# Kernel optimization log

Measured on AMD Instinct MI355X. Metric: run time of the kernel, lower is better.

Reference implementation:

```python
import jax, jax.numpy as jnp
import numpy as np

B, T, C, D = 4, 2048, 48, 512
L = 16                    # transcript length per video (distinct labels)
K = 9                     # bdy_kernel
CS = 15                   # cs_kernel
N_TR = L - 1
N_CAND = 3 * N_TR         # candidate_mul * pt_num
WIN_LEN = int(T / L * 0.15)   # int(t / t_len * win_scale)
ALPHA, BETA, GAMMA, TEMP = 1.0, 1.0, 0.1, 0.1
LOG2 = float(np.log(2.0))

def _bdy_kernel():
    ker = np.zeros((K, K), np.float32)
    c = K // 2
    ker[:c, :c] = 1; ker[c:, c:] = 1
    ker[:c, c:] = -1; ker[c:, :c] = -1
    ker[c, c] = 0
    return jnp.asarray(ker)

BDY_KER = _bdy_kernel()

def bdy_score_fn(prob):
    # prob: [T, C]; sliding windows of size K over time (zero padded)
    c = K // 2
    pad = jnp.pad(prob, ((c, c), (0, 0)))
    win = pad[jnp.arange(T)[:, None] + jnp.arange(K)[None, :]]       # [T,K,C]
    p = win[:, :, None, :]                                           # [T,K,1,C]
    m = (p + win[:, None, :, :]) / 2                                 # [T,K,K,C]
    # torch F.kl_div((m+1e-32).log(), p) = p*(log p - log(m+1e-32)), xlogy(0)=0
    kl = jnp.sum(jnp.where(p > 0, p * (jnp.log(jnp.where(p > 0, p, 1.0)) - jnp.log(m + 1e-32)), 0.0), -1)
    js = (kl + jnp.swapaxes(kl, 1, 2)) / 2
    js = -(js / LOG2 * 2 - 1)                                        # [T,K,K]
    return jnp.mean(BDY_KER[None] * js, axis=(-1, -2))               # [T]

def dp(cls_score):
    # cls_score: [N_TR, N_CAND]; min-cost alignment DP, inner jj-loop vectorized
    cost = -cls_score
    n_tr, n_x = N_TR, N_CAND
    W = 2 * n_tr + 1
    col = jnp.arange(W)
    inf = jnp.float32(jnp.inf)
    tr_at = jnp.clip(col // 2, 0, n_tr - 1)
    even = (col % 2 == 0)
    ge2 = col >= 2

    def init_cols(ii):
        c0 = jnp.where(ii < n_x - n_tr, 0.0, inf)
        c1 = jnp.where(ii <= n_x - n_tr, cost[0, ii], inf)
        d1 = jnp.where(ii <= n_x - n_tr, 1, 0).astype(jnp.int32)
        return c0, c1, d1

    c0, c1, d1 = init_cols(0)
    row0 = jnp.full((W,), inf).at[0].set(c0).at[1].set(c1)
    dir0 = jnp.zeros((W,), jnp.int32).at[1].set(d1)

    def step(prev, ii):
        dm1 = jnp.concatenate([jnp.full((1,), inf), prev[:-1]])
        dm2 = jnp.concatenate([jnp.full((2,), inf), prev[:-2]])
        c_at = cost[:, ii][tr_at]
        even_val = jnp.minimum(prev, dm1)
        even_dir = jnp.where(prev < dm1, 0, 1).astype(jnp.int32)
        odd_val = c_at + jnp.minimum(dm1, dm2)
        odd_dir = jnp.where(dm1 < dm2, 1, 2).astype(jnp.int32)
        c0, c1, d1 = init_cols(ii)
        new = jnp.where(ge2, jnp.where(even, even_val, odd_val), inf)
        new = new.at[0].set(c0).at[1].set(c1)
        dirs = jnp.where(ge2, jnp.where(even, even_dir, odd_dir), 0).astype(jnp.int32)
        dirs = dirs.at[1].set(d1)
        return new, dirs

    last, dirs = jax.lax.scan(step, row0, jnp.arange(1, n_x))
    dir_mat = jnp.concatenate([dir0[None], dirs], 0)                 # [n_x, W]
    cur_j0 = jnp.where(last[2 * n_tr] < last[2 * n_tr - 1], 2 * n_tr, 2 * n_tr - 1).astype(jnp.int32)

    def bt(cur_j, x):
        ii, dir_row = x
        is_odd = (cur_j % 2) == 1
        out_idx = jnp.where(is_odd, cur_j // 2, jnp.int32(n_tr))     # n_tr = OOB -> dropped
        new_j = cur_j - dir_row[cur_j]
        return new_j, (out_idx, ii.astype(jnp.int32))

    _, (oi, ovals) = jax.lax.scan(bt, cur_j0, (jnp.arange(n_x), dir_mat), reverse=True)
    return jnp.zeros((n_tr,), jnp.int32).at[oi].set(ovals, mode='drop')

def detect(logit, tr):
    # logit: [T,C] (detached), tr: [L] ints -> boundary frame indices [N_TR]
    prob = jax.nn.softmax(logit, -1)
    score = bdy_score_fn(prob).at[0].set(-jnp.inf)
    backup = score
    pos = jnp.arange(T)

    def pick(s, _):
        i = jnp.argmax(s)
        return jnp.where(jnp.abs(pos - i) <= WIN_LEN, -jnp.inf, s), i

    _, cand = jax.lax.scan(pick, score, None, length=N_CAND)
    cand = jnp.sort(cand)                                            # [N_CAND]
    # class-transition score at candidate points
    cc = CS // 2
    pairs = jnp.pad(prob[:, tr], ((cc, cc), (0, 0)))                 # [T+2cc, L]
    win = pairs[cand[:, None] + jnp.arange(CS)[None, :]]             # [N_CAND, CS, L]
    first, second = win[:, :, :-1], win[:, :, 1:]
    k0 = jnp.where(jnp.arange(CS) < cc, 1.0, -1.0)[None, :, None]
    cls = jnp.sum(k0 * (first - second), axis=1) / (2 * CS)          # [N_CAND, N_TR]
    cls = cls.T + backup[cand][None, :]                              # [N_TR, N_CAND]
    return cand[dp(cls)]

def _forward(tok_logit, fr_logit, vid_multi_hot, feat, mask, transcript):
    y = vid_multi_hot
    tok_loss = jnp.mean(-(y * jax.nn.log_sigmoid(tok_logit) + (1 - y) * jax.nn.log_sigmoid(-tok_logit)))
    # boundary detection on detached logits
    bdy = jax.vmap(detect)(jax.lax.stop_gradient(fr_logit), transcript)   # [B, N_TR]
    pse = jax.vmap(lambda b, tr: tr[jnp.sum(jnp.arange(T)[:, None] >= b[None, :], axis=1)])(bdy, transcript)
    # frame CE (bgw==1.0 path, full mask so no -100 labels)
    logp = jax.nn.log_softmax(fr_logit, -1)
    ce = -jnp.take_along_axis(logp, pse[..., None], axis=-1)[..., 0]
    m = mask.astype(ce.dtype)
    fr_loss = jnp.sum(ce * m) / jnp.sum(m)
    # global-local contrast
    tok_feat = jax.lax.stop_gradient(feat[:, :C, :])
    fr_feat = feat[:, C:, :]

    def glc_one(tok, fr, pse_i, tr, m_i):
        labels = jnp.sort(tr)                                        # = unique(pse[mask]), distinct labels
        oh = (pse_i[None, :] == labels[:, None]).astype(fr.dtype) * m_i[None, :]
        cnt = jnp.maximum(jnp.sum(oh, 1, keepdims=True), 1.0)
        la = (oh @ fr) / cnt
        la = la / jnp.maximum(jnp.linalg.norm(la, axis=-1, keepdims=True), 1e-12)
        tk = tok / jnp.maximum(jnp.linalg.norm(tok, axis=-1, keepdims=True), 1e-12)
        sim = (la @ tk.T) / TEMP                                     # [L, C]
        return jnp.mean(-jnp.take_along_axis(jax.nn.log_softmax(sim, -1), labels[:, None], axis=-1))

    glc_loss = jnp.mean(jax.vmap(glc_one)(tok_feat, fr_feat, pse, transcript, mask.astype(feat.dtype)))
    return ALPHA * tok_loss + BETA * fr_loss + GAMMA * glc_loss

def setup_inputs() -> dict:
    key = jax.random.key(0)
    ks = jax.random.split(key, 5)
    tok_logit = jax.random.normal(ks[0], (B, C), jnp.float32)
    fr_logit = jax.random.normal(ks[1], (B, T, C), jnp.float32)
    mask = jnp.ones((B, T), bool)
    transcript = jax.vmap(lambda k: jax.random.permutation(k, C)[:L])(jax.random.split(ks[2], B)).astype(jnp.int32)
    vid_multi_hot = jax.random.uniform(ks[3], (B, C), jnp.float32)
    feat = jax.random.normal(ks[4], (B, C + T, D), jnp.float32)
    return {"epoch": 5, "tok_logit": tok_logit, "fr_logit": fr_logit, "mask": mask,
            "transcript": transcript, "vid_multi_hot": vid_multi_hot, "feat": feat}

def reference(epoch, tok_logit, fr_logit, mask, transcript, vid_multi_hot, feat):
    # epoch >= warm_epc (=0), so the full loss path runs
    return _forward(tok_logit, fr_logit, vid_multi_hot, feat, mask, transcript)
```

## Files before the change

kernel.cpp:

```cpp
#include <hip/hip_runtime.h>
#include <math.h>

#define BB 4
#define TT 2048
#define CC 48
#define DD 512
#define LL 16
#define NTR 15
#define NCAND 45
#define WINLEN 19
#define CSW 15
#define CCHALF 7

static __device__ __forceinline__ float wave_reduce_sum(float v) {
    for (int off = 32; off; off >>= 1) v += __shfl_down(v, off);
    return v;
}

#define DPPMAX(x, ctrl) fmaxf((x), __int_as_float(__builtin_amdgcn_update_dpp( \
    __float_as_int(x), __float_as_int(x), (ctrl), 0xF, 0xF, false)))

__global__ __launch_bounds__(256) void k_lse(const float* __restrict__ fr,
                                             float* __restrict__ lse) {
    int row = blockIdx.x * 4 + (threadIdx.x >> 6);
    int lane = threadIdx.x & 63;
    float xv = (lane < CC) ? fr[(size_t)row * CC + lane] : -INFINITY;
    float m = xv;
    for (int off = 32; off; off >>= 1) m = fmaxf(m, __shfl_down(m, off));
    m = __shfl(m, 0);
    float e = (lane < CC) ? __expf(xv - m) : 0.f;
    float s = wave_reduce_sum(e);
    if (lane == 0) lse[row] = m + __logf(s);
}

__global__ __launch_bounds__(64) void k_score(const float* __restrict__ fr,
                                              const float* __restrict__ lse,
                                              float* __restrict__ score) {
    int row = blockIdx.x;
    int b = row / TT, t = row % TT;
    __shared__ float sp[9][CC];
    __shared__ float slp[9][CC];
    __shared__ float lse_s[9];
    int tid = threadIdx.x;
    if (tid < 9) {
        int r = t - 4 + tid;
        lse_s[tid] = (r >= 0 && r < TT) ? lse[b * TT + r] : 0.f;
    }
    __syncthreads();
    for (int idx = tid; idx < 9 * CC; idx += 64) {
        int i = idx / CC, c = idx - (idx / CC) * CC;
        int r = t - 4 + i;
        float pv = 0.f, lv = 0.f;
        if (r >= 0 && r < TT) {
            float x = fr[((size_t)b * TT + r) * CC + c];
            lv = x - lse_s[i];
            pv = __expf(lv);
        }
        sp[i][c] = pv;
        slp[i][c] = lv;
    }
    __syncthreads();
    float acc = 0.f;
    for (int idx = tid; idx < 4 * CC; idx += 64) {
        int i = idx / CC, c = idx - (idx / CC) * CC;
        acc += -2.f * sp[i][c] * slp[i][c];
    }
    for (int item = tid; item < 36 * CC; item += 64) {
        int pidx = item / CC, c = item - pidx * CC;
        int i = 0, rem = pidx;
        while (rem >= 8 - i) { rem -= 8 - i; ++i; }
        int j = i + 1 + rem;
        float wgt = ((i < 4) == (j < 4)) ? 1.f : -1.f;
        float pi = sp[i][c], pj = sp[j][c];
        float logm = __logf(0.5f * (pi + pj) + 1e-32f);
        acc -= wgt * (pi + pj) * logm;
    }
    acc = wave_reduce_sum(acc);
    if (tid == 0) {
        const float SC = -2.0f / (81.0f * 0.6931471805599453f);
        score[row] = (t == 0) ? -INFINITY : SC * acc;
    }
}

__global__ __launch_bounds__(256) void k_pickdp(const float* __restrict__ fr,
                                                const float* __restrict__ lse,
                                                const float* __restrict__ score,
                                                const int* __restrict__ transcript,
                                                int* __restrict__ labels_out,
                                                int* __restrict__ rowmap,
                                                float* __restrict__ fr_part,
                                                float* __restrict__ la) {
    int b = blockIdx.x;
    __shared__ int cl[NCAND];
    __shared__ float cost[NTR][NCAND];
    __shared__ int tr_s[LL];
    __shared__ int cand_s[NCAND];
    __shared__ float backup_s[NCAND];
    __shared__ signed char dir_mat[NCAND][32];
    __shared__ int bdy_s[NTR];
    __shared__ int rank_s[LL];
    __shared__ float rv[2][4];
    __shared__ int rp[2][4];
    __shared__ float redf[4];
    int tid = threadIdx.x;
    int wave = tid >> 6, lane = tid & 63;
    if (tid < LL) tr_s[tid] = transcript[b * LL + tid];

    {
        float4 z = {0.f, 0.f, 0.f, 0.f};
        float4* lz = (float4*)(la + (size_t)b * LL * DD);
        #pragma unroll
        for (int i = 0; i < LL * DD / 4 / 256; ++i) lz[i * 256 + tid] = z;
    }

    float v[8];
    {
        const float4* sp4 = (const float4*)(score + (size_t)b * TT);
        float4 va = sp4[2 * tid], vb = sp4[2 * tid + 1];
        v[0] = va.x; v[1] = va.y; v[2] = va.z; v[3] = va.w;
        v[4] = vb.x; v[5] = vb.y; v[6] = vb.z; v[7] = vb.w;
    }
    for (int it = 0; it < NCAND; ++it) {
        float best = -INFINITY; int bi = 0;
        #pragma unroll
        for (int k = 7; k >= 0; --k)
            if (v[k] >= best) { best = v[k]; bi = k; }
        int pos = tid * 8 + bi;
        float m = best;
        m = DPPMAX(m, 0x111); m = DPPMAX(m, 0x112);
        m = DPPMAX(m, 0x114); m = DPPMAX(m, 0x118);
        m = DPPMAX(m, 0x142); m = DPPMAX(m, 0x143);
        float wmax = __int_as_float(__builtin_amdgcn_readlane(__float_as_int(m), 63));
        unsigned long long ball = __ballot(best == wmax);
        int sl = (int)(__ffsll((long long)ball) - 1);
        int wpos = __builtin_amdgcn_readlane(pos, sl);
        if (lane == 0) { rv[it & 1][wave] = wmax; rp[it & 1][wave] = wpos; }
        __syncthreads();
        float bvv = -INFINITY; int mp = 0x7fffffff;
        #pragma unroll
        for (int w = 0; w < 4; ++w) {
            float vv = rv[it & 1][w]; int pp = rp[it & 1][w];
            if (vv > bvv || (vv == bvv && pp < mp)) { bvv = vv; mp = pp; }
        }
        if (tid == 0) cl[it] = mp;
        int lo = mp - WINLEN, hi = mp + WINLEN;
        #pragma unroll
        for (int k = 0; k < 8; ++k) {
            int t = tid * 8 + k;
            if (t >= lo && t <= hi) v[k] = -INFINITY;
        }
    }
    __syncthreads();
    if (tid < NCAND) {
        int my = cl[tid];
        int rank = 0;
        for (int i = 0; i < NCAND; ++i) rank += (cl[i] < my) ? 1 : 0;
        cand_s[rank] = my;
    }
    __syncthreads();
    if (tid < NCAND) backup_s[tid] = score[(size_t)b * TT + cand_s[tid]];
    __syncthreads();

    for (int e = tid; e < NTR * NCAND; e += 256) {
        int j = e / NCAND, ii = e - (e / NCAND) * NCAND;
        int cpos = cand_s[ii];
        int trj = tr_s[j], trj1 = tr_s[j + 1];
        float sum = 0.f;
        #pragma unroll
        for (int k = 0; k < CSW; ++k) {
            int r = cpos - CCHALF + k;
            float a = 0.f, d2 = 0.f;
            if (r >= 0 && r < TT) {
                size_t ro = (size_t)b * TT + r;
                float ls = lse[ro];
                a  = __expf(fr[ro * CC + trj]  - ls);
                d2 = __expf(fr[ro * CC + trj1] - ls);
            }
            sum += ((k < CCHALF) ? 1.f : -1.f) * (a - d2);
        }
        cost[j][ii] = -(sum / 30.f + backup_s[ii]);
    }
    __syncthreads();

    if (tid < 64) {
        float prev = INFINITY;
        if (tid == 0) prev = 0.f;
        if (tid == 1) prev = cost[0][0];
        if (tid < 31) dir_mat[0][tid] = (tid == 1) ? (signed char)1 : (signed char)0;
        for (int ii = 1; ii < NCAND; ++ii) {
            float dm1 = __shfl_up(prev, 1); if (tid < 1) dm1 = INFINITY;
            float dm2 = __shfl_up(prev, 2); if (tid < 2) dm2 = INFINITY;
            int trat = tid >> 1; if (trat > NTR - 1) trat = NTR - 1;
            float c_at = cost[trat][ii];
            float ev = fminf(prev, dm1);
            int ed = (prev < dm1) ? 0 : 1;
            float ov = c_at + fminf(dm1, dm2);
            int od = (dm1 < dm2) ? 1 : 2;
            float nv; int nd;
            if (tid >= 2) {
                if ((tid & 1) == 0) { nv = ev; nd = ed; }
                else { nv = ov; nd = od; }
            } else { nv = INFINITY; nd = 0; }
            if (tid == 0) { nv = (ii < NCAND - NTR) ? 0.f : INFINITY; nd = 0; }
            if (tid == 1) {
                nv = (ii <= NCAND - NTR) ? cost[0][ii] : INFINITY;
                nd = (ii <= NCAND - NTR) ? 1 : 0;
            }
            prev = nv;
            if (tid < 31) dir_mat[ii][tid] = (signed char)nd;
        }
        float v29 = __shfl(prev, 29);
        float v30 = __shfl(prev, 30);
        if (tid == 0) {
            int cur = (v30 < v29) ? 30 : 29;
            for (int ii = NCAND - 1; ii >= 0; --ii) {
                if (cur & 1) bdy_s[cur >> 1] = cand_s[ii];
                cur -= (int)dir_mat[ii][cur];
            }
        }
    }
    __syncthreads();

    if (tid < LL) {
        int myv = tr_s[tid];
        int r2 = 0;
        #pragma unroll
        for (int l2 = 0; l2 < LL; ++l2) r2 += (tr_s[l2] < myv) ? 1 : 0;
        rank_s[tid] = r2;
        labels_out[b * LL + r2] = myv;
    }
    __syncthreads();

    float facc = 0.f;
    for (int t = tid; t < TT; t += 256) {
        int cnt = 0;
        #pragma unroll
        for (int j = 0; j < NTR; ++j) cnt += (t >= bdy_s[j]) ? 1 : 0;
        int pv = tr_s[cnt];
        rowmap[b * TT + t] = rank_s[cnt];
        size_t ro = (size_t)b * TT + t;
        facc += lse[ro] - fr[ro * CC + pv];
    }
    facc = wave_reduce_sum(facc);
    if (lane == 0) redf[wave] = facc;
    __syncthreads();
    if (tid == 0) fr_part[b] = redf[0] + redf[1] + redf[2] + redf[3];
}

__global__ __launch_bounds__(256) void k_la(const float* __restrict__ feat,
                                            const int* __restrict__ rowmap,
                                            float* __restrict__ la) {
    int b = blockIdx.y;
    int t0 = blockIdx.x * 32;
    int tid = threadIdx.x;
    const float* frf = feat + ((size_t)b * (CC + TT) + CC) * DD;
    __shared__ int rm[32];
    if (tid < 32) rm[tid] = rowmap[b * TT + t0 + tid];
    __syncthreads();
    float ax = 0.f, ay = 0.f;
    int cur = rm[0];
    for (int k = 0; k < 32; ++k) {
        int r = rm[k];
        if (r != cur) {
            float* dst = la + ((size_t)b * LL + cur) * DD + tid * 2;
            atomicAdd(dst, ax);
            atomicAdd(dst + 1, ay);
            ax = 0.f; ay = 0.f; cur = r;
        }
        const float2* p = (const float2*)(frf + (size_t)(t0 + k) * DD);
        float2 v = p[tid];
        ax += v.x; ay += v.y;
    }
    float* dst = la + ((size_t)b * LL + cur) * DD + tid * 2;
    atomicAdd(dst, ax);
    atomicAdd(dst + 1, ay);
}

__global__ __launch_bounds__(256) void k_glc(const float* __restrict__ feat,
                                             const float* __restrict__ la,
                                             float* __restrict__ dots,
                                             float* __restrict__ ntk) {
    int c = blockIdx.x, b = blockIdx.y;
    __shared__ float tok_s[DD];
    __shared__ float redv[4];
    int tid = threadIdx.x;
    int wave = tid >> 6, lane = tid & 63;
    const float* tr = feat + ((size_t)b * (CC + TT) + c) * DD;
    float2 tv = ((const float2*)tr)[tid];
    ((float2*)tok_s)[tid] = tv;
    float vv = tv.x * tv.x + tv.y * tv.y;
    vv = wave_reduce_sum(vv);
    if (lane == 0) redv[wave] = vv;
    __syncthreads();
    if (tid == 0)
        ntk[b * CC + c] = fmaxf(sqrtf(redv[0] + redv[1] + redv[2] + redv[3]), 1e-12f);
    for (int l = wave; l < LL; l += 4) {
        const float4* lar = (const float4*)(la + ((size_t)b * LL + l) * DD);
        const float4* ts = (const float4*)tok_s;
        float dot = 0.f;
        #pragma unroll
        for (int jj = 0; jj < 2; ++jj) {
            int j = lane + jj * 64;
            float4 a = lar[j]; float4 w = ts[j];
            dot += a.x * w.x + a.y * w.y + a.z * w.z + a.w * w.w;
        }
        dot = wave_reduce_sum(dot);
        if (lane == 0) dots[((size_t)b * LL + l) * CC + c] = dot;
    }
}

__global__ __launch_bounds__(64) void k_term(const float* __restrict__ la,
                                             const float* __restrict__ dots,
                                             const float* __restrict__ ntk,
                                             const int* __restrict__ labels,
                                             float* __restrict__ terms) {
    int l = blockIdx.x, b = blockIdx.y;
    int lane = threadIdx.x;
    const float4* lar = (const float4*)(la + ((size_t)b * LL + l) * DD);
    float ss = 0.f;
    #pragma unroll
    for (int jj = 0; jj < 2; ++jj) {
        float4 a = lar[lane + jj * 64];
        ss += a.x * a.x + a.y * a.y + a.z * a.z + a.w * a.w;
    }
    ss = wave_reduce_sum(ss);
    float nla = fmaxf(sqrtf(__shfl(ss, 0)), 1e-12f);
    float sim = -INFINITY;
    if (lane < CC)
        sim = dots[((size_t)b * LL + l) * CC + lane] * 10.0f / (nla * ntk[b * CC + lane]);
    float mx = sim;
    for (int off = 32; off; off >>= 1) mx = fmaxf(mx, __shfl_down(mx, off));
    mx = __shfl(mx, 0);
    float e = (lane < CC) ? expf(sim - mx) : 0.f;
    float se = wave_reduce_sum(e);
    se = __shfl(se, 0);
    int lab = labels[b * LL + l];
    float sim_lab = __shfl(sim, lab);
    if (lane == 0) terms[b * LL + l] = (mx + logf(se)) - sim_lab;
}

__global__ __launch_bounds__(256) void k_combine(const float* __restrict__ tok_logit,
                                                 const float* __restrict__ vid,
                                                 const float* __restrict__ fr_part,
                                                 const float* __restrict__ terms,
                                                 float* __restrict__ out) {
    int tid = threadIdx.x;
    __shared__ float red[4];
    __shared__ float gterm;
    float acc = 0.f;
    if (tid < BB * CC) {
        float x = tok_logit[tid], y = vid[tid];
        float lsp = fminf(x, 0.f) - log1pf(expf(-fabsf(x)));
        float lsn = fminf(-x, 0.f) - log1pf(expf(-fabsf(x)));
        acc = -(y * lsp + (1.f - y) * lsn);
    }
    float w = wave_reduce_sum(acc);
    if ((tid & 63) == 0) red[tid >> 6] = w;
    if (tid < 64) {
        float g = terms[tid];
        g = wave_reduce_sum(g);
        if (tid == 0) gterm = g;
    }
    __syncthreads();
    if (tid == 0) {
        float s_tok = (red[0] + red[1] + red[2] + red[3]) / (float)(BB * CC);
        float sfr = fr_part[0] + fr_part[1] + fr_part[2] + fr_part[3];
        float s_fr = sfr / (float)(BB * TT);
        float glc = gterm / (float)(BB * LL);
        out[0] = s_tok + s_fr + 0.1f * glc;
    }
}

extern "C" void kernel_launch(void* const* d_in, const int* in_sizes, int n_in,
                              void* d_out, int out_size, void* d_ws, size_t ws_size,
                              hipStream_t stream) {
    (void)in_sizes; (void)n_in; (void)out_size; (void)ws_size;
    const float* tok_logit  = (const float*)d_in[1];
    const float* fr_logit   = (const float*)d_in[2];
    const int*   transcript = (const int*)d_in[4];
    const float* vid        = (const float*)d_in[5];
    const float* feat       = (const float*)d_in[6];

    char* ws = (char*)d_ws;
    float* lse     = (float*)(ws + 0);
    float* score   = (float*)(ws + 32768);
    float* la      = (float*)(ws + 65536);
    float* dots    = (float*)(ws + 196608);
    float* ntk     = (float*)(ws + 208896);
    float* terms   = (float*)(ws + 209664);
    float* fr_part = (float*)(ws + 209920);
    int*   labels  = (int*)(ws + 210176);
    int*   rowmap  = (int*)(ws + 210432);
    float* out     = (float*)d_out;

    k_lse<<<BB * TT / 4, 256, 0, stream>>>(fr_logit, lse);
    k_score<<<BB * TT, 64, 0, stream>>>(fr_logit, lse, score);
    k_pickdp<<<BB, 256, 0, stream>>>(fr_logit, lse, score, transcript,
                                     labels, rowmap, fr_part, la);
    k_la<<<dim3(TT / 32, BB), 256, 0, stream>>>(feat, rowmap, la);
    k_glc<<<dim3(CC, BB), 256, 0, stream>>>(feat, la, dots, ntk);
    k_term<<<dim3(LL, BB), 64, 0, stream>>>(la, dots, ntk, labels, terms);
    k_combine<<<1, 256, 0, stream>>>(tok_logit, vid, fr_part, terms, out);
}
```

Baseline: 171.3 us.

## Split candidate picking into single-wave kernel to remove per-iteration block barriers

Moves the 45-step iterative argmax-with-suppression out of the 256-thread DP kernel into its own kernel, which uses one 64-lane wave holding 32 scores per lane. This removes the __syncthreads and cross-wave shared-memory reduction from every iteration and uses a bitmask to suppress the window. The cost is an extra kernel launch and a global round trip for the candidates and their backup scores, plus each lane scanning 32 values per iteration instead of 8.

```diff
diff --git a/kernel.cpp b/kernel.cpp
--- a/kernel.cpp
+++ b/kernel.cpp
@@ -82,16 +82,62 @@
     }
 }
 
-__global__ __launch_bounds__(256) void k_pickdp(const float* __restrict__ fr,
-                                                const float* __restrict__ lse,
-                                                const float* __restrict__ score,
-                                                const int* __restrict__ transcript,
-                                                int* __restrict__ labels_out,
-                                                int* __restrict__ rowmap,
-                                                float* __restrict__ fr_part,
-                                                float* __restrict__ la) {
+__global__ __launch_bounds__(64) void k_pick(const float* __restrict__ score,
+                                             int* __restrict__ cand,
+                                             float* __restrict__ backup) {
     int b = blockIdx.x;
+    int lane = threadIdx.x;
+    __shared__ float s[64 * 33];
     __shared__ int cl[NCAND];
+    for (int t = lane; t < TT; t += 64) s[t + (t >> 5)] = score[(size_t)b * TT + t];
+    __syncthreads();
+    float v[32];
+    #pragma unroll
+    for (int k = 0; k < 32; ++k) v[k] = s[lane * 33 + k];
+    int base = lane << 5;
+    for (int it = 0; it < NCAND; ++it) {
+        float best = -INFINITY; int bi = 0;
+        #pragma unroll
+        for (int k = 31; k >= 0; --k)
+            if (v[k] >= best) { best = v[k]; bi = k; }
+        float m = best;
+        m = DPPMAX(m, 0x111); m = DPPMAX(m, 0x112);
+        m = DPPMAX(m, 0x114); m = DPPMAX(m, 0x118);
+        m = DPPMAX(m, 0x142); m = DPPMAX(m, 0x143);
+        float gmax = __int_as_float(__builtin_amdgcn_readlane(__float_as_int(m), 63));
+        unsigned long long ball = __ballot(best == gmax);
+        int sl = (int)(__ffsll((long long)ball) - 1);
+        int mp = __builtin_amdgcn_readlane(base + bi, sl);
+        if (lane == 0) cl[it] = mp;
+        int llo = mp - WINLEN - base;
+        int lhi = mp + WINLEN - base;
+        unsigned lowm = (llo <= 0) ? 0xffffffffu : ((llo >= 32) ? 0u : ~((1u << llo) - 1u));
+        unsigned him  = (lhi >= 31) ? 0xffffffffu : ((lhi < 0) ? 0u : ((2u << lhi) - 1u));
+        unsigned wm = lowm & him;
+        #pragma unroll
+        for (int k = 0; k < 32; ++k)
+            if (wm & (1u << k)) v[k] = -INFINITY;
+    }
+    __syncthreads();
+    if (lane < NCAND) {
+        int my = cl[lane];
+        int rank = 0;
+        for (int i = 0; i < NCAND; ++i) rank += (cl[i] < my) ? 1 : 0;
+        cand[b * 64 + rank] = my;
+        backup[b * 64 + rank] = s[my + (my >> 5)];
+    }
+}
+
+__global__ __launch_bounds__(256) void k_dp(const float* __restrict__ fr,
+                                            const float* __restrict__ lse,
+                                            const int* __restrict__ cand,
+                                            const float* __restrict__ backup,
+                                            const int* __restrict__ transcript,
+                                            int* __restrict__ labels_out,
+                                            int* __restrict__ rowmap,
+                                            float* __restrict__ fr_part,
+                                            float* __restrict__ la) {
+    int b = blockIdx.x;
     __shared__ float cost[NTR][NCAND];
     __shared__ int tr_s[LL];
     __shared__ int cand_s[NCAND];
@@ -99,12 +145,14 @@
     __shared__ signed char dir_mat[NCAND][32];
     __shared__ int bdy_s[NTR];
     __shared__ int rank_s[LL];
-    __shared__ float rv[2][4];
-    __shared__ int rp[2][4];
     __shared__ float redf[4];
     int tid = threadIdx.x;
     int wave = tid >> 6, lane = tid & 63;
     if (tid < LL) tr_s[tid] = transcript[b * LL + tid];
+    if (tid < NCAND) {
+        cand_s[tid] = cand[b * 64 + tid];
+        backup_s[tid] = backup[b * 64 + tid];
+    }
 
     {
         float4 z = {0.f, 0.f, 0.f, 0.f};
@@ -112,53 +160,6 @@
         #pragma unroll
         for (int i = 0; i < LL * DD / 4 / 256; ++i) lz[i * 256 + tid] = z;
     }
-
-    float v[8];
-    {
-        const float4* sp4 = (const float4*)(score + (size_t)b * TT);
-        float4 va = sp4[2 * tid], vb = sp4[2 * tid + 1];
-        v[0] = va.x; v[1] = va.y; v[2] = va.z; v[3] = va.w;
-        v[4] = vb.x; v[5] = vb.y; v[6] = vb.z; v[7] = vb.w;
-    }
-    for (int it = 0; it < NCAND; ++it) {
-        float best = -INFINITY; int bi = 0;
-        #pragma unroll
-        for (int k = 7; k >= 0; --k)
-            if (v[k] >= best) { best = v[k]; bi = k; }
-        int pos = tid * 8 + bi;
-        float m = best;
-        m = DPPMAX(m, 0x111); m = DPPMAX(m, 0x112);
-        m = DPPMAX(m, 0x114); m = DPPMAX(m, 0x118);
-        m = DPPMAX(m, 0x142); m = DPPMAX(m, 0x143);
-        float wmax = __int_as_float(__builtin_amdgcn_readlane(__float_as_int(m), 63));
-        unsigned long long ball = __ballot(best == wmax);
-        int sl = (int)(__ffsll((long long)ball) - 1);
-        int wpos = __builtin_amdgcn_readlane(pos, sl);
-        if (lane == 0) { rv[it & 1][wave] = wmax; rp[it & 1][wave] = wpos; }
-        __syncthreads();
-        float bvv = -INFINITY; int mp = 0x7fffffff;
-        #pragma unroll
-        for (int w = 0; w < 4; ++w) {
-            float vv = rv[it & 1][w]; int pp = rp[it & 1][w];
-            if (vv > bvv || (vv == bvv && pp < mp)) { bvv = vv; mp = pp; }
-        }
-        if (tid == 0) cl[it] = mp;
-        int lo = mp - WINLEN, hi = mp + WINLEN;
-        #pragma unroll
-        for (int k = 0; k < 8; ++k) {
-            int t = tid * 8 + k;
-            if (t >= lo && t <= hi) v[k] = -INFINITY;
-        }
-    }
-    __syncthreads();
-    if (tid < NCAND) {
-        int my = cl[tid];
-        int rank = 0;
-        for (int i = 0; i < NCAND; ++i) rank += (cl[i] < my) ? 1 : 0;
-        cand_s[rank] = my;
-    }
-    __syncthreads();
-    if (tid < NCAND) backup_s[tid] = score[(size_t)b * TT + cand_s[tid]];
     __syncthreads();
 
     for (int e = tid; e < NTR * NCAND; e += 256) {
@@ -391,12 +392,15 @@
     float* fr_part = (float*)(ws + 209920);
     int*   labels  = (int*)(ws + 210176);
     int*   rowmap  = (int*)(ws + 210432);
+    int*   cand    = (int*)(ws + 243200);
+    float* backup  = (float*)(ws + 244224);
     float* out     = (float*)d_out;
 
     k_lse<<<BB * TT / 4, 256, 0, stream>>>(fr_logit, lse);
     k_score<<<BB * TT, 64, 0, stream>>>(fr_logit, lse, score);
-    k_pickdp<<<BB, 256, 0, stream>>>(fr_logit, lse, score, transcript,
-                                     labels, rowmap, fr_part, la);
+    k_pick<<<BB, 64, 0, stream>>>(score, cand, backup);
+    k_dp<<<BB, 256, 0, stream>>>(fr_logit, lse, cand, backup, transcript,
+                                 labels, rowmap, fr_part, la);
     k_la<<<dim3(TT / 32, BB), 256, 0, stream>>>(feat, rowmap, la);
     k_glc<<<dim3(CC, BB), 256, 0, stream>>>(feat, la, dots, ntk);
     k_term<<<dim3(LL, BB), 64, 0, stream>>>(la, dots, ntk, labels, terms);
```

Measured after the change: 171.6 us. About the same (+0.2%).
